# Kernel tuning notes

Measured on AMD Instinct MI355X. Metric: run time of the kernel, lower is better.

Reference implementation:

```python
import jax, jax.numpy as jnp
import numpy as np

N = 4096   # nodes
D = 512    # feature dim
E = 65536  # edges
HOPS = 10  # APPNP K (init arg 'hops')
ALPHA = 0.5


def setup_inputs() -> dict:
    key = jax.random.key(0)
    k1, k2, k3 = jax.random.split(key, 3)
    x_train = jax.random.normal(k1, (N, D), dtype=jnp.float32)
    # kernel_scale = nn.Linear(D, 1, bias=False) weight, flattened to [D]
    w = jax.random.normal(k2, (D,), dtype=jnp.float32) * 0.05
    edge_index = jax.random.randint(k3, (2, E), 0, N, dtype=jnp.int32)
    return {"x_train": x_train, "w": w, "edge_index": edge_index}


def appnp(x0, src, dst, hops, alpha):
    # torch_geometric APPNP with gcn_norm (add self-loops, symmetric norm), dropout=0
    n = x0.shape[0]
    loop = jnp.arange(n, dtype=src.dtype)
    s = jnp.concatenate([src, loop])
    d = jnp.concatenate([dst, loop])
    deg = jax.ops.segment_sum(jnp.ones_like(s, dtype=x0.dtype), d, num_segments=n)
    dis = deg ** -0.5  # deg >= 1 thanks to self-loops
    norm = dis[s] * dis[d]

    def body(h, _):
        agg = jax.ops.segment_sum(norm[:, None] * h[s], d, num_segments=n)
        return (1.0 - alpha) * agg + alpha * x0, None

    h, _ = jax.lax.scan(body, x0, None, length=hops)
    return h


def reference(x_train, w, edge_index):
    n = x_train.shape[0]
    # RBF_kernel: K[i,j] = sum_d w_d * (x_i - x_j)_d^2 for i != j, diag = 1 (the eye)
    xw = x_train * w                                   # [N, D]
    sq = jnp.sum(xw * x_train, axis=1)                 # [N] weighted squared norms
    K = sq[:, None] + sq[None, :] - 2.0 * (xw @ x_train.T)  # [N, N]
    idx = jnp.arange(n)
    K = K.at[idx, idx].set(1.0)

    src, dst = edge_index[0], edge_index[1]
    kgg = appnp(K, src, dst, HOPS, ALPHA)
    kgg = appnp(kgg.T, src, dst, HOPS, ALPHA)

    # adj = dense coo(edge_index, ones); diag = (diag(adj.sum(dim=1)) + 1) ** -0.5
    # (adds 1 to the WHOLE matrix, so off-diagonal entries become 1.0 -- faithful)
    deg_row = jax.ops.segment_sum(jnp.ones((edge_index.shape[1],), K.dtype), src, num_segments=n)
    Dmat = (jnp.diag(deg_row) + 1.0) ** -0.5           # [N, N]
    kgg = Dmat * kgg       # elementwise, as in the original
    kgg = Dmat * kgg.T
    return kgg
```

## Files before the change

### kernel.cpp

```cpp
#include <hip/hip_runtime.h>
#include <stdint.h>

#define Nn 4096
#define Dd 512
#define Ee 65536
#define HOPS 10
#define TPB 512
#define RPT (Nn / TPB)
#define CT8 8
#define WCAP 64
#define KEXT 1536
#define YC 640
#define XK 8192

typedef short bf16x8 __attribute__((ext_vector_type(8)));
typedef float f32x4 __attribute__((ext_vector_type(4)));

__device__ __forceinline__ unsigned short bf16r(float x) {
  unsigned int b = __float_as_uint(x);
  return (unsigned short)((b + 0x7FFFu + ((b >> 16) & 1u)) >> 16);
}
__device__ __forceinline__ unsigned int pkbf(float lo, float hi) {
  return (unsigned int)bf16r(lo) | ((unsigned int)bf16r(hi) << 16);
}
__device__ __forceinline__ float ubf(unsigned short h) {
  return __uint_as_float(((unsigned int)h) << 16);
}
__device__ __forceinline__ void gld16(const unsigned short* g, unsigned short* lds) {
  __builtin_amdgcn_global_load_lds(
      (const __attribute__((address_space(1))) unsigned int*)g,
      (__attribute__((address_space(3))) unsigned int*)lds, 16, 0, 0);
}

__global__ __launch_bounds__(256) void k_sq(const float* __restrict__ x,
                                            const float* __restrict__ w,
                                            float* __restrict__ sq) {
  int row = blockIdx.x;
  int tid = threadIdx.x;
  const float* xr = x + (size_t)row * Dd;
  float partial = 0.f;
  for (int d = tid; d < Dd; d += 256) {
    float xv = xr[d];
    partial += xv * xv * w[d];
  }
  for (int off = 32; off >= 1; off >>= 1) partial += __shfl_down(partial, off, 64);
  __shared__ float red[4];
  int wv = tid >> 6, ln = tid & 63;
  if (ln == 0) red[wv] = partial;
  __syncthreads();
  if (tid == 0) sq[row] = red[0] + red[1] + red[2] + red[3];
}

__global__ void k_count(const int* __restrict__ src, const int* __restrict__ dst,
                        int* __restrict__ degi, int* __restrict__ degrow) {
  int e = blockIdx.x * blockDim.x + threadIdx.x;
  if (e < Ee) {
    atomicAdd(&degi[dst[e]], 1);
    atomicAdd(&degrow[src[e]], 1);
  }
}

__global__ void k_dis(const int* __restrict__ degi, const int* __restrict__ degrow,
                      float* __restrict__ dis, float* __restrict__ d2) {
  int i = blockIdx.x * 256 + threadIdx.x;
  dis[i] = rsqrtf((float)(degi[i] + 1));
  d2[i] = 1.0f / ((float)degrow[i] + 1.0f);
}

__global__ void k_hist(const int* __restrict__ degi, int* __restrict__ binbase) {
  __shared__ int h[WCAP + 1];
  int t = threadIdx.x;
  if (t <= WCAP) h[t] = 0;
  __syncthreads();
  for (int i = t; i < Nn; i += 256) {
    int d = degi[i] + 1;
    if (d > WCAP) d = WCAP;
    atomicAdd(&h[d], 1);
  }
  __syncthreads();
  if (t == 0) {
    int run = 0;
    for (int b = 0; b <= WCAP; b++) { int c = h[b]; binbase[b] = run; run += c; }
  }
}

__global__ void k_scatter(const int* __restrict__ degi, const int* __restrict__ binbase,
                          int* __restrict__ bincnt, int* __restrict__ perm,
                          int* __restrict__ rnk) {
  int i = blockIdx.x * 256 + threadIdx.x;
  int d = degi[i] + 1;
  if (d > WCAP) d = WCAP;
  int pos = binbase[d] + atomicAdd(&bincnt[d], 1);
  perm[pos] = i;
  rnk[i] = pos;
}

__global__ void k_wsub(const int* __restrict__ degi, const int* __restrict__ perm,
                       int* __restrict__ wsub) {
  int t = threadIdx.x;
  int d = degi[perm[t * 64 + 63]] + 1;
  wsub[t] = d > WCAP ? WCAP : d;
}

__global__ void k_fill_ell(const int* __restrict__ src, const int* __restrict__ dst,
                           const float* __restrict__ dis, const int* __restrict__ rnk,
                           int* __restrict__ slot, int2* __restrict__ ell) {
  int i = blockIdx.x * blockDim.x + threadIdx.x;
  if (i < Ee) {
    int s = src[i], d = dst[i];
    int p = atomicAdd(&slot[d], 1);
    if (p < WCAP) ell[(size_t)p * Nn + rnk[d]] = make_int2(s, __float_as_int(dis[s] * dis[d]));
  } else if (i < Ee + Nn) {
    int v = i - Ee;
    int p = atomicAdd(&slot[v], 1);
    if (p < WCAP) ell[(size_t)p * Nn + rnk[v]] = make_int2(v, __float_as_int(dis[v] * dis[v]));
  }
}

__global__ __launch_bounds__(256) void k_xpose(const float* __restrict__ x,
                                               unsigned short* __restrict__ xb) {
  __shared__ float tile[32][33];
  int cx = blockIdx.x, rx = blockIdx.y;
  int t = threadIdx.x, txc = t & 31, tyc = t >> 5;
#pragma unroll
  for (int i = 0; i < 4; i++) {
    int a = tyc + i * 8;
    tile[a][txc] = x[(size_t)(rx * 32 + a) * Dd + cx * 32 + txc];
  }
  __syncthreads();
#pragma unroll
  for (int i = 0; i < 4; i++) {
    int a = tyc + i * 8;
    int c = cx * 32 + a;
    float v = tile[txc][a];
    unsigned short hi = bf16r(v);
    xb[(size_t)c * XK + rx * 32 + txc] = hi;
    xb[(size_t)c * XK + Nn + rx * 32 + txc] = bf16r(v - ubf(hi));
  }
}

__global__ void k_tail(const float* __restrict__ sq, unsigned short* __restrict__ xb) {
  int r = blockIdx.x * 256 + threadIdx.x;
  float v = sq[r];
  unsigned short hi = bf16r(v);
  xb[(size_t)512 * XK + r] = hi;
  xb[(size_t)512 * XK + Nn + r] = bf16r(v - ubf(hi));
  xb[(size_t)513 * XK + r] = bf16r(1.0f);
  xb[(size_t)513 * XK + Nn + r] = 0;
}

__global__ __launch_bounds__(TPB, 4) void k_appnp(unsigned short* __restrict__ mb,
                                                  const int2* __restrict__ ell,
                                                  const int* __restrict__ perm,
                                                  const int* __restrict__ wsub) {
  extern __shared__ uint4 h4u[];
  int j0 = blockIdx.x * CT8;
  int tid = threadIdx.x;
  int wv = tid >> 6, ln = tid & 63;
  int qb = wv * 512 + ln;

#pragma unroll
  for (int rr = 0; rr < RPT; rr++) {
    int r = tid + rr * TPB;
    uint4 v = make_uint4(0u, 0u, 0u, 0u);
    int c = r - j0;
    if (c >= 0 && c < 8) {
      unsigned int one = (c & 1) ? 0x3F800000u : 0x00003F80u;
      if ((c >> 1) == 0) v.x = one;
      else if ((c >> 1) == 1) v.y = one;
      else if ((c >> 1) == 2) v.z = one;
      else v.w = one;
    }
    h4u[r] = v;
  }

  int ws[RPT];
#pragma unroll
  for (int rr = 0; rr < RPT; rr++)
    ws[rr] = __builtin_amdgcn_readfirstlane(wsub[wv * 8 + rr]);
  const int Wv = ws[RPT - 1];

  int rp[RPT], x0c[RPT];
#pragma unroll
  for (int rr = 0; rr < RPT; rr++) {
    rp[rr] = perm[qb + rr * 64];
    int c = rp[rr] - j0;
    x0c[rr] = (c >= 0 && c < 8) ? c : -1;
  }
  __syncthreads();

  for (int it = 0; it < HOPS; it++) {
    int2 cur[RPT];
#pragma unroll
    for (int rr = 0; rr < RPT; rr++) cur[rr] = ell[qb + rr * 64];
    float acc[RPT][8];
#pragma unroll
    for (int rr = 0; rr < RPT; rr++)
#pragma unroll
      for (int c = 0; c < 8; c++) acc[rr][c] = (x0c[rr] == c) ? 1.0f : 0.0f;
    for (int s = 0; s < Wv; s++) {
      int sn = s + 1;
      int2 nxt[RPT];
#pragma unroll
      for (int rr = 0; rr < RPT; rr++)
        if (sn < ws[rr]) nxt[rr] = ell[(size_t)sn * Nn + qb + rr * 64];
#pragma unroll
      for (int rr = 0; rr < RPT; rr++)
        if (s < ws[rr]) {
          float vv = __int_as_float(cur[rr].y);
          uint4 hu = h4u[cur[rr].x];
          acc[rr][0] = fmaf(vv, __uint_as_float(hu.x << 16), acc[rr][0]);
          acc[rr][1] = fmaf(vv, __uint_as_float(hu.x & 0xFFFF0000u), acc[rr][1]);
          acc[rr][2] = fmaf(vv, __uint_as_float(hu.y << 16), acc[rr][2]);
          acc[rr][3] = fmaf(vv, __uint_as_float(hu.y & 0xFFFF0000u), acc[rr][3]);
          acc[rr][4] = fmaf(vv, __uint_as_float(hu.z << 16), acc[rr][4]);
          acc[rr][5] = fmaf(vv, __uint_as_float(hu.z & 0xFFFF0000u), acc[rr][5]);
          acc[rr][6] = fmaf(vv, __uint_as_float(hu.w << 16), acc[rr][6]);
          acc[rr][7] = fmaf(vv, __uint_as_float(hu.w & 0xFFFF0000u), acc[rr][7]);
        }
#pragma unroll
      for (int rr = 0; rr < RPT; rr++)
        if (sn < ws[rr]) cur[rr] = nxt[rr];
    }
    __syncthreads();
#pragma unroll
    for (int rr = 0; rr < RPT; rr++) {
      uint4 v;
      v.x = pkbf(0.5f * acc[rr][0], 0.5f * acc[rr][1]);
      v.y = pkbf(0.5f * acc[rr][2], 0.5f * acc[rr][3]);
      v.z = pkbf(0.5f * acc[rr][4], 0.5f * acc[rr][5]);
      v.w = pkbf(0.5f * acc[rr][6], 0.5f * acc[rr][7]);
      h4u[rp[rr]] = v;
    }
    __syncthreads();
  }

#pragma unroll
  for (int rr = 0; rr < RPT; rr++) {
    int r = tid + rr * TPB;
    *(uint4*)&mb[(size_t)r * Nn + j0] = h4u[r];
  }
}

__device__ __forceinline__ void mm_step(const unsigned short* __restrict__ Ap, int lda,
                                        const unsigned short* __restrict__ Bp, int ldb,
                                        unsigned short* As, unsigned short* Bs,
                                        int i0, int j0, int k0, int l, int w, int wr,
                                        int wc, f32x4 acc[4][4]) {
  int rsub = w * 8 + (l >> 3);
  int scg = ((l & 7) ^ (l >> 3)) * 8;
#pragma unroll
  for (int r = 0; r < 4; r++) {
    int row = r * 32 + rsub;
    gld16(Ap + (size_t)(i0 + row) * lda + k0 + scg, As + (r * 32 + w * 8) * 64);
    gld16(Bp + (size_t)(j0 + row) * ldb + k0 + scg, Bs + (r * 32 + w * 8) * 64);
  }
  __syncthreads();
#pragma unroll
  for (int q = 0; q < 2; q++) {
    bf16x8 af[4], bg[4];
#pragma unroll
    for (int m = 0; m < 4; m++) {
      int ar = wr * 64 + m * 16 + (l & 15);
      af[m] = *(const bf16x8*)(As + ar * 64 + ((((l >> 4) + 4 * q) ^ (ar & 7)) * 8));
      int br = wc * 64 + m * 16 + (l & 15);
      bg[m] = *(const bf16x8*)(Bs + br * 64 + ((((l >> 4) + 4 * q) ^ (br & 7)) * 8));
    }
#pragma unroll
    for (int m = 0; m < 4; m++)
#pragma unroll
      for (int n = 0; n < 4; n++)
        acc[m][n] = __builtin_amdgcn_mfma_f32_16x16x32_bf16(af[m], bg[n], acc[m][n], 0, 0, 0);
  }
  __syncthreads();
}

__global__ __launch_bounds__(256) void k_ymm(const unsigned short* __restrict__ Mb,
                                             const unsigned short* __restrict__ xb,
                                             const float* __restrict__ wp,
                                             unsigned short* __restrict__ aext,
                                             unsigned short* __restrict__ bext,
                                             float* __restrict__ mu,
                                             float* __restrict__ m1) {
  __shared__ unsigned short As[128 * 64];
  __shared__ unsigned short Bs[128 * 64];
  int i0 = blockIdx.y * 128, j0 = blockIdx.x * 128;
  int tid = threadIdx.x, l = tid & 63, w = tid >> 6;
  int wr = w >> 1, wc = w & 1;
  f32x4 acc[4][4];
#pragma unroll
  for (int m = 0; m < 4; m++)
#pragma unroll
    for (int n = 0; n < 4; n++) acc[m][n] = (f32x4){0.f, 0.f, 0.f, 0.f};

  for (int k0 = 0; k0 < Nn; k0 += 64)
    mm_step(Mb, Nn, xb, XK, As, Bs, i0, j0, k0, l, w, wr, wc, acc);
  for (int k0 = 0; k0 < Nn; k0 += 64)
    mm_step(Mb, Nn, xb + Nn, XK, As, Bs, i0, j0, k0, l, w, wr, wc, acc);

#pragma unroll
  for (int m = 0; m < 4; m++) {
#pragma unroll
    for (int n = 0; n < 4; n++) {
#pragma unroll
      for (int q = 0; q < 4; q++) {
        int gi = i0 + wr * 64 + m * 16 + ((l >> 4) << 2) + q;
        int gj = j0 + wc * 64 + n * 16 + (l & 15);
        float y = acc[m][n][q];
        if (gj < 512) {
          unsigned short yhi = bf16r(y);
          unsigned short ylo = bf16r(y - ubf(yhi));
          float p = -2.f * wp[gj] * y;
          unsigned short phi = bf16r(p);
          unsigned short plo = bf16r(p - ubf(phi));
          bext[(size_t)gi * KEXT + gj] = yhi;
          bext[(size_t)gi * KEXT + 512 + gj] = ylo;
          bext[(size_t)gi * KEXT + 1024 + gj] = yhi;
          aext[(size_t)gi * KEXT + gj] = phi;
          aext[(size_t)gi * KEXT + 512 + gj] = phi;
          aext[(size_t)gi * KEXT + 1024 + gj] = plo;
        } else if (gj == 512) {
          mu[gi] = y;
        } else if (gj == 513) {
          m1[gi] = y;
        }
      }
    }
  }
}

__global__ __launch_bounds__(256) void k_mm(const unsigned short* __restrict__ Mb,
                                            const unsigned short* __restrict__ Aext,
                                            const unsigned short* __restrict__ Bext,
                                            const float* __restrict__ mu,
                                            const float* __restrict__ m1,
                                            const float* __restrict__ d2,
                                            float* __restrict__ out) {
  __shared__ unsigned short As[128 * 64];
  __shared__ unsigned short Bs[128 * 64];
  int lid = blockIdx.y * 32 + blockIdx.x;
  int swz = (lid & 7) * 128 + (lid >> 3);
  int i0 = (swz >> 5) * 128, j0 = (swz & 31) * 128;
  int tid = threadIdx.x, l = tid & 63, w = tid >> 6;
  int wr = w >> 1, wc = w & 1;
  f32x4 acc[4][4];
#pragma unroll
  for (int m = 0; m < 4; m++)
#pragma unroll
    for (int n = 0; n < 4; n++) acc[m][n] = (f32x4){0.f, 0.f, 0.f, 0.f};

  for (int k0 = 0; k0 < Nn; k0 += 64)
    mm_step(Mb, Nn, Mb, Nn, As, Bs, i0, j0, k0, l, w, wr, wc, acc);
  for (int k0 = 0; k0 < KEXT; k0 += 64)
    mm_step(Aext, KEXT, Bext, KEXT, As, Bs, i0, j0, k0, l, w, wr, wc, acc);

#pragma unroll
  for (int m = 0; m < 4; m++) {
#pragma unroll
    for (int n = 0; n < 4; n++) {
#pragma unroll
      for (int q = 0; q < 4; q++) {
        int gi = i0 + wr * 64 + m * 16 + ((l >> 4) << 2) + q;
        int gj = j0 + wc * 64 + n * 16 + (l & 15);
        float v = acc[m][n][q] + mu[gi] * m1[gj] + m1[gi] * mu[gj];
        if (gi == gj) v *= d2[gi];
        out[(size_t)gi * Nn + gj] = v;
      }
    }
  }
}

extern "C" void kernel_launch(void* const* d_in, const int* in_sizes, int n_in,
                              void* d_out, int out_size, void* d_ws, size_t ws_size,
                              hipStream_t stream) {
  const float* x = (const float*)d_in[0];
  const float* w = (const float*)d_in[1];
  const int* ei = (const int*)d_in[2];
  const int* src = ei;
  const int* dstv = ei + Ee;
  float* out = (float*)d_out;

  unsigned short* Mb = (unsigned short*)d_ws;
  unsigned short* aext = Mb + (size_t)Nn * Nn;
  unsigned short* bext = aext + (size_t)Nn * KEXT;
  unsigned short* xb = bext + (size_t)Nn * KEXT;
  int2* ell = (int2*)(xb + (size_t)YC * XK);
  float* sq = (float*)(ell + (size_t)WCAP * Nn);
  float* dis = sq + Nn;
  float* d2 = dis + Nn;
  float* mu = d2 + Nn;
  float* m1 = mu + Nn;
  int* degi = (int*)(m1 + Nn);
  int* degrow = degi + Nn;
  int* slotcnt = degrow + Nn;
  int* bincnt = slotcnt + Nn;
  int* binbase = bincnt + (WCAP + 1);
  int* perm = binbase + (WCAP + 1);
  int* rnk = perm + Nn;
  int* wsub = rnk + Nn;

  hipMemsetAsync(ell, 0, (size_t)WCAP * Nn * sizeof(int2), stream);
  hipMemsetAsync(degi, 0, sizeof(int) * (3 * Nn + (WCAP + 1)), stream);
  hipMemsetAsync(xb, 0, (size_t)YC * XK * sizeof(unsigned short), stream);

  k_sq<<<Nn, 256, 0, stream>>>(x, w, sq);
  k_count<<<Ee / 256, 256, 0, stream>>>(src, dstv, degi, degrow);
  k_dis<<<Nn / 256, 256, 0, stream>>>(degi, degrow, dis, d2);
  k_hist<<<1, 256, 0, stream>>>(degi, binbase);
  k_scatter<<<Nn / 256, 256, 0, stream>>>(degi, binbase, bincnt, perm, rnk);
  k_wsub<<<1, 64, 0, stream>>>(degi, perm, wsub);
  k_fill_ell<<<(Ee + Nn + 255) / 256, 256, 0, stream>>>(src, dstv, dis, rnk, slotcnt, ell);
  k_xpose<<<dim3(16, 128), 256, 0, stream>>>(x, xb);
  k_tail<<<Nn / 256, 256, 0, stream>>>(sq, xb);

  k_appnp<<<Nn / CT8, TPB, Nn * sizeof(uint4), stream>>>(Mb, ell, perm, wsub);
  k_ymm<<<dim3(YC / 128, Nn / 128), 256, 0, stream>>>(Mb, xb, w, aext, bext, mu, m1);
  k_mm<<<dim3(32, 32), 256, 0, stream>>>(Mb, aext, bext, mu, m1, d2, out);
}
```

Before: 891.7 us.

## Rewrite final GEMM with 256x256 tiles, double-buffered LDS and interleaved prefetch

Replaces the 128x128-tile final bf16 GEMM with a 256x256-tile, 512-thread kernel that double-buffers A/B tiles in 128KB of dynamic LDS using direct global-to-LDS loads. It uses an XOR-swizzled layout to avoid bank conflicts, splits each k-step into four phases that interleave prefetch issue with MFMA work, and raises wave priority around the MFMAs. The goal is more data reuse per global byte and overlap of loads with compute. The cost is heavier register and LDS pressure and only 256 blocks, which may leave some CUs underused.

```diff
diff --git a/kernel.cpp b/kernel.cpp
--- a/kernel.cpp
+++ b/kernel.cpp
@@ -12,6 +12,7 @@
 #define KEXT 1536
 #define YC 640
 #define XK 8192
+#define NTMM 88
 
 typedef short bf16x8 __attribute__((ext_vector_type(8)));
 typedef float f32x4 __attribute__((ext_vector_type(4)));
@@ -329,38 +330,104 @@
   }
 }
 
-__global__ __launch_bounds__(256) void k_mm(const unsigned short* __restrict__ Mb,
-                                            const unsigned short* __restrict__ Aext,
-                                            const unsigned short* __restrict__ Bext,
-                                            const float* __restrict__ mu,
-                                            const float* __restrict__ m1,
-                                            const float* __restrict__ d2,
-                                            float* __restrict__ out) {
-  __shared__ unsigned short As[128 * 64];
-  __shared__ unsigned short Bs[128 * 64];
-  int lid = blockIdx.y * 32 + blockIdx.x;
-  int swz = (lid & 7) * 128 + (lid >> 3);
-  int i0 = (swz >> 5) * 128, j0 = (swz & 31) * 128;
+__global__ __launch_bounds__(512, 2) void k_mm2(const unsigned short* __restrict__ Mb,
+                                                const unsigned short* __restrict__ Aext,
+                                                const unsigned short* __restrict__ Bext,
+                                                const float* __restrict__ mu,
+                                                const float* __restrict__ m1,
+                                                const float* __restrict__ d2,
+                                                float* __restrict__ out) {
+  extern __shared__ unsigned short sh[];
+  int lid = blockIdx.x;
+  int swz = (lid & 7) * 32 + (lid >> 3);
+  int i0 = (swz >> 4) * 256, j0 = (swz & 15) * 256;
   int tid = threadIdx.x, l = tid & 63, w = tid >> 6;
-  int wr = w >> 1, wc = w & 1;
-  f32x4 acc[4][4];
-#pragma unroll
-  for (int m = 0; m < 4; m++)
+  int wr = w >> 2, wc = w & 3;
+  int rsub = l >> 3;
+  int scg = ((l & 7) ^ (l >> 3)) * 8;
+  int aRowBase = wr * 128 + wc * 32;
+  int bRowBase = (wc >> 1) * 128 + (wr * 2 + (wc & 1)) * 32;
+
+  f32x4 acc[8][4];
+#pragma unroll
+  for (int m = 0; m < 8; m++)
 #pragma unroll
     for (int n = 0; n < 4; n++) acc[m][n] = (f32x4){0.f, 0.f, 0.f, 0.f};
 
-  for (int k0 = 0; k0 < Nn; k0 += 64)
-    mm_step(Mb, Nn, Mb, Nn, As, Bs, i0, j0, k0, l, w, wr, wc, acc);
-  for (int k0 = 0; k0 < KEXT; k0 += 64)
-    mm_step(Aext, KEXT, Bext, KEXT, As, Bs, i0, j0, k0, l, w, wr, wc, acc);
-
-#pragma unroll
-  for (int m = 0; m < 4; m++) {
+  auto STG = [&](int g, int t, int b) {
+    const unsigned short *pa, *pb;
+    int lda, kk;
+    if (t < 64) { pa = Mb; pb = Mb; lda = Nn; kk = t * 64; }
+    else { pa = Aext; pb = Bext; lda = KEXT; kk = (t - 64) * 64; }
+    if (g < 4) {
+      int r = bRowBase + g * 8;
+      gld16(pb + (size_t)(j0 + r + rsub) * lda + kk + scg, sh + 32768 + b * 16384 + r * 64);
+    } else {
+      int r = aRowBase + (g - 4) * 8;
+      gld16(pa + (size_t)(i0 + r + rsub) * lda + kk + scg, sh + b * 16384 + r * 64);
+    }
+  };
+
+#pragma unroll
+  for (int g = 0; g < 8; g++) STG(g, 0, 0);
+  asm volatile("s_waitcnt vmcnt(0)" ::: "memory");
+  __builtin_amdgcn_s_barrier();
+
+  for (int kt = 0; kt < NTMM; kt++) {
+    int cur = kt & 1, nxtb = cur ^ 1;
+    const unsigned short* Ac = sh + cur * 16384;
+    const unsigned short* Bc = sh + 32768 + cur * 16384;
+    bool pre = (kt + 1 < NTMM);
+#pragma unroll
+    for (int p = 0; p < 4; p++) {
+      const int mh = p >> 1, nh = p & 1;
+      bf16x8 af[4][2], bg[2][2];
+#pragma unroll
+      for (int m4 = 0; m4 < 4; m4++) {
+        int ar = wr * 128 + (mh * 4 + m4) * 16 + (l & 15);
+#pragma unroll
+        for (int ks = 0; ks < 2; ks++) {
+          int c = ks * 4 + (l >> 4);
+          af[m4][ks] = *(const bf16x8*)(Ac + ar * 64 + ((c ^ (ar & 7)) * 8));
+        }
+      }
+#pragma unroll
+      for (int n2 = 0; n2 < 2; n2++) {
+        int br = wc * 64 + (nh * 2 + n2) * 16 + (l & 15);
+#pragma unroll
+        for (int ks = 0; ks < 2; ks++) {
+          int c = ks * 4 + (l >> 4);
+          bg[n2][ks] = *(const bf16x8*)(Bc + br * 64 + ((c ^ (br & 7)) * 8));
+        }
+      }
+      if (pre) {
+        if (p == 0) { STG(0, kt + 1, nxtb); STG(1, kt + 1, nxtb); STG(2, kt + 1, nxtb); }
+        else if (p == 1) { STG(3, kt + 1, nxtb); STG(4, kt + 1, nxtb); STG(5, kt + 1, nxtb); }
+        else if (p == 2) { STG(6, kt + 1, nxtb); STG(7, kt + 1, nxtb); }
+      }
+      if (p == 3) asm volatile("s_waitcnt vmcnt(0)" ::: "memory");
+      __builtin_amdgcn_s_barrier();
+      __builtin_amdgcn_s_setprio(1);
+#pragma unroll
+      for (int m4 = 0; m4 < 4; m4++)
+#pragma unroll
+        for (int n2 = 0; n2 < 2; n2++)
+#pragma unroll
+          for (int ks = 0; ks < 2; ks++)
+            acc[mh * 4 + m4][nh * 2 + n2] = __builtin_amdgcn_mfma_f32_16x16x32_bf16(
+                af[m4][ks], bg[n2][ks], acc[mh * 4 + m4][nh * 2 + n2], 0, 0, 0);
+      __builtin_amdgcn_s_setprio(0);
+      __builtin_amdgcn_s_barrier();
+    }
+  }
+
+#pragma unroll
+  for (int m = 0; m < 8; m++) {
 #pragma unroll
     for (int n = 0; n < 4; n++) {
 #pragma unroll
       for (int q = 0; q < 4; q++) {
-        int gi = i0 + wr * 64 + m * 16 + ((l >> 4) << 2) + q;
+        int gi = i0 + wr * 128 + m * 16 + ((l >> 4) << 2) + q;
         int gj = j0 + wc * 64 + n * 16 + (l & 15);
         float v = acc[m][n][q] + mu[gi] * m1[gj] + m1[gi] * mu[gj];
         if (gi == gj) v *= d2[gi];
@@ -415,5 +482,5 @@
 
   k_appnp<<<Nn / CT8, TPB, Nn * sizeof(uint4), stream>>>(Mb, ell, perm, wsub);
   k_ymm<<<dim3(YC / 128, Nn / 128), 256, 0, stream>>>(Mb, xb, w, aext, bext, mu, m1);
-  k_mm<<<dim3(32, 32), 256, 0, stream>>>(Mb, aext, bext, mu, m1, d2, out);
-}
+  k_mm2<<<256, 512, 131072, stream>>>(Mb, aext, bext, mu, m1, d2, out);
+}
```

Result: faster. 865.8 us (-2.9%).
